# Kernel optimization log

Measured on AMD Instinct MI355X. Metric: run time of the kernel, lower is better.

The kernel has to match this reference:

```python
import jax, jax.numpy as jnp
import numpy as np

VOCAB = 50000
SEQ = 2048
BATCH = 64
D = 256


def setup_inputs() -> dict:
    key = jax.random.key(0)
    ks = jax.random.split(key, 9)
    x = jax.random.randint(ks[0], (SEQ, BATCH), 0, VOCAB)  # token ids, 0 = pad
    emb = jax.random.normal(ks[1], (VOCAB, D), jnp.float32) * 0.02
    emb = emb.at[0].set(0.0)  # padding_idx=0
    idf = jax.random.uniform(ks[2], (VOCAB,), jnp.float32, 0.1, 10.0)
    W1 = jax.random.normal(ks[3], (100, D), jnp.float32) * (1.0 / np.sqrt(D))
    b1 = jax.random.normal(ks[4], (100,), jnp.float32) * 0.01
    W2 = jax.random.normal(ks[5], (150, 100), jnp.float32) * 0.1
    b2 = jax.random.normal(ks[6], (150,), jnp.float32) * 0.01
    W3 = jax.random.normal(ks[7], (2, 150), jnp.float32) * 0.1
    b3 = jax.random.normal(ks[8], (2,), jnp.float32) * 0.01
    return {"x": x, "emb": emb, "idf": idf, "W1": W1, "b1": b1,
            "W2": W2, "b2": b2, "W3": W3, "b3": b3}


def reference(x, emb, idf, W1, b1, W2, b2, W3, b3):
    tokens = x.T  # [B, S] (nums = x.permute(1, 0))
    vocab = emb.shape[0]

    # per-row term frequency: histogram (scatter-add) then gather back
    def tf_row(row):  # row: [S] int
        return jnp.zeros((vocab,), jnp.float32).at[row].add(1.0)[row]

    tf = jax.vmap(tf_row)(tokens)                      # [B, S]
    scores = jnp.where(tokens == 0, 0.0, tf * idf[tokens])  # [B, S]

    # bmm of (B, D, S) with (B, S, 1) == tf-idf weighted sum of embeddings
    pooled = jnp.einsum('bsd,bs->bd', emb[tokens], scores)  # [B, D]

    h = jax.nn.relu(pooled @ W1.T + b1)
    h = jax.nn.relu(h @ W2.T + b2)
    return jax.nn.softmax(h @ W3.T + b3, axis=-1)  # [B, 2]
```

## Files before the change

### kernel.cpp

```cpp
#include <hip/hip_runtime.h>

#define VOCAB 50000
#define SEQ   2048
#define BATCH 64
#define DIM   256
#define H1    100
#define H2    150
#define HASH  4096
#define NCH   8
#define CHUNK (SEQ / NCH)
#define NT    1024
#define NWAVE (NT / 64)

__global__ __launch_bounds__(1024)
void k_gather(const int* __restrict__ x,
              const float* __restrict__ emb,
              const float* __restrict__ idf,
              float* __restrict__ partials) {
    __shared__ int   tok[SEQ];
    __shared__ int   hkey[HASH];
    __shared__ int   hcnt[HASH];
    __shared__ float sc[CHUNK];
    __shared__ float wacc[NWAVE][DIM];

    const int bx = blockIdx.x;
    const int r  = bx >> 3;
    const int c  = bx & (NCH - 1);
    const int t  = threadIdx.x;
    const int w  = t >> 6, lane = t & 63;
    const int s0 = c * CHUNK;

    for (int i = t; i < HASH; i += NT) { hkey[i] = -1; hcnt[i] = 0; }
#pragma unroll
    for (int n = 0; n < SEQ / NT; ++n) {
        const int s = n * NT + t;
        tok[s] = x[s * BATCH + r];
    }
    __syncthreads();

#pragma unroll
    for (int n = 0; n < SEQ / NT; ++n) {
        const int s = n * NT + t;
        const int mytok = tok[s];
        unsigned h = ((unsigned)mytok * 2654435761u) >> 20;
        while (true) {
            int prev = atomicCAS(&hkey[h], -1, mytok);
            if (prev == -1 || prev == mytok) { atomicAdd(&hcnt[h], 1); break; }
            h = (h + 1) & (HASH - 1);
        }
    }
    __syncthreads();

    if (t < CHUNK) {
        const int s = s0 + t;
        const int mytok = tok[s];
        unsigned h = ((unsigned)mytok * 2654435761u) >> 20;
        while (hkey[h] != mytok) h = (h + 1) & (HASH - 1);
        sc[t] = (mytok == 0) ? 0.0f : (float)hcnt[h] * idf[mytok];
    }
    __syncthreads();

    {
        const float4* embv = (const float4*)emb;
        float4 acc = make_float4(0.f, 0.f, 0.f, 0.f);
        const int i0 = w * (CHUNK / NWAVE);
#pragma unroll
        for (int i = 0; i < CHUNK / NWAVE; ++i) {
            const float sv = sc[i0 + i];
            const float4 v = embv[(size_t)tok[s0 + i0 + i] * (DIM / 4) + lane];
            acc.x = fmaf(v.x, sv, acc.x);
            acc.y = fmaf(v.y, sv, acc.y);
            acc.z = fmaf(v.z, sv, acc.z);
            acc.w = fmaf(v.w, sv, acc.w);
        }
        ((float4*)wacc[w])[lane] = acc;
    }
    __syncthreads();

    if (t < DIM) {
        float a = 0.0f;
#pragma unroll
        for (int i = 0; i < NWAVE; ++i) a += wacc[i][t];
        partials[(size_t)bx * DIM + t] = a;
    }
}

__global__ __launch_bounds__(1024)
void k_mlp(const float* __restrict__ partials,
           const float* __restrict__ W1, const float* __restrict__ b1,
           const float* __restrict__ W2, const float* __restrict__ b2,
           const float* __restrict__ W3, const float* __restrict__ b3,
           float* __restrict__ out) {
    __shared__ float pooled[DIM];
    __shared__ float hp1[128][4];
    __shared__ float h1s[112];
    __shared__ float hp2[H2][4];
    __shared__ float h2s[152];
    __shared__ float lg[2];
    const int r = blockIdx.x;
    const int t = threadIdx.x;

    if (t < DIM) {
        float a = 0.0f;
#pragma unroll
        for (int cc = 0; cc < NCH; ++cc)
            a += partials[((size_t)r * NCH + cc) * DIM + t];
        pooled[t] = a;
    }
    __syncthreads();

    if (t < 512) {
        const int j = t >> 2;
        const int q = t & 3;
        if (j < H1) {
            const float4* wv = (const float4*)(W1 + j * DIM + q * 64);
            const float4* pv = ((const float4*)pooled) + q * 16;
            float a = 0.0f;
#pragma unroll
            for (int i = 0; i < 16; ++i) {
                const float4 ww = wv[i];
                const float4 pp = pv[i];
                a += ww.x * pp.x + ww.y * pp.y + ww.z * pp.z + ww.w * pp.w;
            }
            hp1[j][q] = a;
        }
    }
    __syncthreads();
    if (t < H1)
        h1s[t] = fmaxf(hp1[t][0] + hp1[t][1] + hp1[t][2] + hp1[t][3] + b1[t], 0.0f);
    __syncthreads();

    if (t < 600) {
        const int j = t >> 2;
        const int q = t & 3;
        const float* wv = W2 + j * H1 + q * 25;
        float a = 0.0f;
#pragma unroll
        for (int i = 0; i < 25; ++i)
            a = fmaf(wv[i], h1s[q * 25 + i], a);
        hp2[j][q] = a;
    }
    __syncthreads();
    if (t < H2)
        h2s[t] = fmaxf(hp2[t][0] + hp2[t][1] + hp2[t][2] + hp2[t][3] + b2[t], 0.0f);
    __syncthreads();

    if (t < 2) {
        const float* wv = W3 + t * H2;
        float a = b3[t];
        for (int k = 0; k < H2; ++k) a = fmaf(wv[k], h2s[k], a);
        lg[t] = a;
    }
    __syncthreads();
    if (t == 0) {
        const float m  = fmaxf(lg[0], lg[1]);
        const float e0 = __expf(lg[0] - m);
        const float e1 = __expf(lg[1] - m);
        const float inv = 1.0f / (e0 + e1);
        out[r * 2 + 0] = e0 * inv;
        out[r * 2 + 1] = e1 * inv;
    }
}

extern "C" void kernel_launch(void* const* d_in, const int* in_sizes, int n_in,
                              void* d_out, int out_size, void* d_ws, size_t ws_size,
                              hipStream_t stream) {
    const int*   x   = (const int*)  d_in[0];
    const float* emb = (const float*)d_in[1];
    const float* idf = (const float*)d_in[2];
    const float* W1  = (const float*)d_in[3];
    const float* b1  = (const float*)d_in[4];
    const float* W2  = (const float*)d_in[5];
    const float* b2  = (const float*)d_in[6];
    const float* W3  = (const float*)d_in[7];
    const float* b3  = (const float*)d_in[8];
    float* out = (float*)d_out;

    float* partials = (float*)d_ws;

    k_gather<<<BATCH * NCH, NT, 0, stream>>>(x, emb, idf, partials);
    k_mlp   <<<BATCH, NT, 0, stream>>>(partials, W1, b1, W2, b2, W3, b3, out);
}
```

Measured before the change: 127.1 us.

## Pack hash key and count into one word, enlarge table, unroll gather

Replaces the separate key/count shared hash arrays with a single 32-bit word holding the token id in the low 16 bits and the count in the high 16 bits. The table doubles in size to reduce probe chains, and the insert uses a read-then-CAS scheme with fetch-add on the count. Only the block's chunk of tokens is kept in shared memory, and the embedding gather uses four independent accumulators to expose more loads in flight. It relies on token ids fitting in 16 bits and on counts staying below 65536.

```diff
diff --git a/kernel.cpp b/kernel.cpp
--- a/kernel.cpp
+++ b/kernel.cpp
@@ -6,22 +6,22 @@
 #define DIM   256
 #define H1    100
 #define H2    150
-#define HASH  4096
+#define HASH  8192
+#define EMPTY 0xFFFFFFFFu
 #define NCH   8
 #define CHUNK (SEQ / NCH)
 #define NT    1024
 #define NWAVE (NT / 64)
 
-__global__ __launch_bounds__(1024)
+__global__ __launch_bounds__(1024, 8)
 void k_gather(const int* __restrict__ x,
               const float* __restrict__ emb,
               const float* __restrict__ idf,
               float* __restrict__ partials) {
-    __shared__ int   tok[SEQ];
-    __shared__ int   hkey[HASH];
-    __shared__ int   hcnt[HASH];
-    __shared__ float sc[CHUNK];
-    __shared__ float wacc[NWAVE][DIM];
+    __shared__ unsigned hh[HASH];
+    __shared__ int      tokc[CHUNK];
+    __shared__ float    sc[CHUNK];
+    __shared__ float    wacc[NWAVE][DIM];
 
     const int bx = blockIdx.x;
     const int r  = bx >> 3;
@@ -30,49 +30,73 @@
     const int w  = t >> 6, lane = t & 63;
     const int s0 = c * CHUNK;
 
-    for (int i = t; i < HASH; i += NT) { hkey[i] = -1; hcnt[i] = 0; }
+#pragma unroll
+    for (int n = 0; n < HASH / NT; ++n) hh[n * NT + t] = EMPTY;
+    if (t < CHUNK) tokc[t] = x[(s0 + t) * BATCH + r];
+    __syncthreads();
+
 #pragma unroll
     for (int n = 0; n < SEQ / NT; ++n) {
         const int s = n * NT + t;
-        tok[s] = x[s * BATCH + r];
-    }
-    __syncthreads();
-
-#pragma unroll
-    for (int n = 0; n < SEQ / NT; ++n) {
-        const int s = n * NT + t;
-        const int mytok = tok[s];
-        unsigned h = ((unsigned)mytok * 2654435761u) >> 20;
+        const unsigned mytok = (unsigned)x[s * BATCH + r];
+        unsigned h = (mytok * 2654435761u) >> 19;
         while (true) {
-            int prev = atomicCAS(&hkey[h], -1, mytok);
-            if (prev == -1 || prev == mytok) { atomicAdd(&hcnt[h], 1); break; }
+            const unsigned cur = hh[h];
+            if ((cur & 0xFFFFu) == mytok) {
+                atomicAdd(&hh[h], 1u << 16);
+                break;
+            }
+            if (cur == EMPTY) {
+                const unsigned prev = atomicCAS(&hh[h], EMPTY, (1u << 16) | mytok);
+                if (prev == EMPTY) break;
+                if ((prev & 0xFFFFu) == mytok) { atomicAdd(&hh[h], 1u << 16); break; }
+                continue;
+            }
             h = (h + 1) & (HASH - 1);
         }
     }
     __syncthreads();
 
     if (t < CHUNK) {
-        const int s = s0 + t;
-        const int mytok = tok[s];
-        unsigned h = ((unsigned)mytok * 2654435761u) >> 20;
-        while (hkey[h] != mytok) h = (h + 1) & (HASH - 1);
-        sc[t] = (mytok == 0) ? 0.0f : (float)hcnt[h] * idf[mytok];
+        const unsigned mytok = (unsigned)tokc[t];
+        unsigned h = (mytok * 2654435761u) >> 19;
+        while ((hh[h] & 0xFFFFu) != mytok) h = (h + 1) & (HASH - 1);
+        const float cnt = (float)(hh[h] >> 16);
+        sc[t] = (mytok == 0u) ? 0.0f : cnt * idf[mytok];
     }
     __syncthreads();
 
     {
         const float4* embv = (const float4*)emb;
-        float4 acc = make_float4(0.f, 0.f, 0.f, 0.f);
+        float4 a0 = make_float4(0.f, 0.f, 0.f, 0.f);
+        float4 a1 = make_float4(0.f, 0.f, 0.f, 0.f);
+        float4 a2 = make_float4(0.f, 0.f, 0.f, 0.f);
+        float4 a3 = make_float4(0.f, 0.f, 0.f, 0.f);
         const int i0 = w * (CHUNK / NWAVE);
 #pragma unroll
-        for (int i = 0; i < CHUNK / NWAVE; ++i) {
-            const float sv = sc[i0 + i];
-            const float4 v = embv[(size_t)tok[s0 + i0 + i] * (DIM / 4) + lane];
-            acc.x = fmaf(v.x, sv, acc.x);
-            acc.y = fmaf(v.y, sv, acc.y);
-            acc.z = fmaf(v.z, sv, acc.z);
-            acc.w = fmaf(v.w, sv, acc.w);
+        for (int i = 0; i < CHUNK / NWAVE; i += 4) {
+            const int   t0 = tokc[i0 + i + 0], t1 = tokc[i0 + i + 1];
+            const int   t2 = tokc[i0 + i + 2], t3 = tokc[i0 + i + 3];
+            const float s0v = sc[i0 + i + 0], s1v = sc[i0 + i + 1];
+            const float s2v = sc[i0 + i + 2], s3v = sc[i0 + i + 3];
+            const float4 v0 = embv[(size_t)t0 * (DIM / 4) + lane];
+            const float4 v1 = embv[(size_t)t1 * (DIM / 4) + lane];
+            const float4 v2 = embv[(size_t)t2 * (DIM / 4) + lane];
+            const float4 v3 = embv[(size_t)t3 * (DIM / 4) + lane];
+            a0.x = fmaf(v0.x, s0v, a0.x); a0.y = fmaf(v0.y, s0v, a0.y);
+            a0.z = fmaf(v0.z, s0v, a0.z); a0.w = fmaf(v0.w, s0v, a0.w);
+            a1.x = fmaf(v1.x, s1v, a1.x); a1.y = fmaf(v1.y, s1v, a1.y);
+            a1.z = fmaf(v1.z, s1v, a1.z); a1.w = fmaf(v1.w, s1v, a1.w);
+            a2.x = fmaf(v2.x, s2v, a2.x); a2.y = fmaf(v2.y, s2v, a2.y);
+            a2.z = fmaf(v2.z, s2v, a2.z); a2.w = fmaf(v2.w, s2v, a2.w);
+            a3.x = fmaf(v3.x, s3v, a3.x); a3.y = fmaf(v3.y, s3v, a3.y);
+            a3.z = fmaf(v3.z, s3v, a3.z); a3.w = fmaf(v3.w, s3v, a3.w);
         }
+        float4 acc;
+        acc.x = (a0.x + a1.x) + (a2.x + a3.x);
+        acc.y = (a0.y + a1.y) + (a2.y + a3.y);
+        acc.z = (a0.z + a1.z) + (a2.z + a3.z);
+        acc.w = (a0.w + a1.w) + (a2.w + a3.w);
         ((float4*)wacc[w])[lane] = acc;
     }
     __syncthreads();
```

Result: no change. 127.9 us (+0.7%).
